# Performance work log

Hardware: AMD Instinct MI355X
Metric: run time of the kernel (lower is better)

## Reference

```python
import jax, jax.numpy as jnp
import numpy as np

B, F, H = 16384, 2048, 4096   # batch, n_features, n_hidden
D, K = 4096, 2048             # num_of_demos, num_of_features


def setup_inputs() -> dict:
    key = jax.random.key(0)
    ks = jax.random.split(key, 16)
    s = 0.02
    return {
        "x": jax.random.normal(ks[0], (B, F), jnp.float32),
        "demo_metric": jax.random.uniform(ks[1], (D, K), jnp.float32),
        "alpha": jax.random.normal(ks[2], (K,), jnp.float32),
        "sample_loss": jax.random.uniform(ks[3], (D, K), jnp.float32),
        "subdom_constant": jax.random.uniform(ks[4], (1,), jnp.float32),
        "num_of_demos": D,
        "num_of_features": K,
        "W1": jax.random.normal(ks[5], (F, H), jnp.float32) * s,
        "b1": jnp.zeros((H,), jnp.float32),
        "W2": jax.random.normal(ks[6], (H, H), jnp.float32) * s,
        "b2": jnp.zeros((H,), jnp.float32),
        "W3": jax.random.normal(ks[7], (H, H), jnp.float32) * s,
        "b3": jnp.zeros((H,), jnp.float32),
        "W4": jax.random.normal(ks[8], (H, 2), jnp.float32) * s,
        "b4": jnp.zeros((2,), jnp.float32),
    }


def reference(x, demo_metric, alpha, sample_loss, subdom_constant,
              num_of_demos, num_of_features,
              W1, b1, W2, b2, W3, b3, W4, b4):
    # subdom hinge loss: max(alpha_k * (sample_loss_jk - demo_loss_jk) + 1, 0) - c
    margin = alpha[None, :] * (sample_loss - demo_metric) + 1.0  # [D, K]
    subdom = jnp.maximum(margin, 0.0) - subdom_constant          # broadcast c
    loss = jnp.sum(subdom)

    # MLP classifier (dropout = identity at inference) + sigmoid
    h = jax.nn.relu(x @ W1 + b1)
    h = jax.nn.relu(h @ W2 + b2)
    h = jax.nn.relu(h @ W3 + b3)
    probs = jax.nn.sigmoid(h @ W4 + b4)  # [B, 2]
    return (loss, probs)
```

## Files before the change

### kernel.cpp

```cpp
#include <hip/hip_runtime.h>
#include <cstdint>
#include <cstddef>

typedef unsigned short u16;
typedef __attribute__((ext_vector_type(8))) __bf16 bf16x8;
typedef __attribute__((ext_vector_type(4))) float f32x4;

__device__ __forceinline__ u16 f2bf(float f) {
  union { float f; unsigned u; } v; v.f = f;
  unsigned r = v.u + 0x7FFFu + ((v.u >> 16) & 1u);
  return (u16)(r >> 16);
}
__device__ __forceinline__ float bf2f(unsigned h) {
  union { unsigned u; float f; } v; v.u = h << 16;
  return v.f;
}

__global__ void init_loss_kernel(const float* __restrict__ c,
                                 const int* __restrict__ D,
                                 const int* __restrict__ K,
                                 float* __restrict__ out) {
  out[0] = -c[0] * (float)D[0] * (float)K[0];
}

__global__ void subdom_kernel(const float4* __restrict__ dm,
                              const float4* __restrict__ sl,
                              const float4* __restrict__ alpha4,
                              float* __restrict__ out, int n4, int k4mask) {
  const int stride = gridDim.x * blockDim.x;
  float s = 0.f;
  for (int i = blockIdx.x * blockDim.x + threadIdx.x; i < n4; i += stride) {
    float4 d = dm[i], l = sl[i], a = alpha4[i & k4mask];
    s += fmaxf(fmaf(a.x, l.x - d.x, 1.f), 0.f);
    s += fmaxf(fmaf(a.y, l.y - d.y, 1.f), 0.f);
    s += fmaxf(fmaf(a.z, l.z - d.z, 1.f), 0.f);
    s += fmaxf(fmaf(a.w, l.w - d.w, 1.f), 0.f);
  }
#pragma unroll
  for (int off = 32; off > 0; off >>= 1) s += __shfl_down(s, off, 64);
  __shared__ float red[4];
  const int lane = threadIdx.x & 63, wave = threadIdx.x >> 6;
  if (lane == 0) red[wave] = s;
  __syncthreads();
  if (threadIdx.x == 0) atomicAdd(out, red[0] + red[1] + red[2] + red[3]);
}

__global__ void cast_f32_bf16_kernel(const float4* __restrict__ in,
                                     u16* __restrict__ out, int n4) {
  const int stride = gridDim.x * blockDim.x;
  for (int i = blockIdx.x * blockDim.x + threadIdx.x; i < n4; i += stride) {
    float4 v = in[i];
    uint2 p;
    p.x = (unsigned)f2bf(v.x) | ((unsigned)f2bf(v.y) << 16);
    p.y = (unsigned)f2bf(v.z) | ((unsigned)f2bf(v.w) << 16);
    ((uint2*)out)[i] = p;
  }
}

__global__ void transpose_cast_kernel(const float* __restrict__ in,
                                      u16* __restrict__ out, int K, int N) {
  __shared__ float tile[32][33];
  const int bx = blockIdx.x * 32;
  const int by = blockIdx.y * 32;
  const int tx = threadIdx.x, ty = threadIdx.y;
#pragma unroll
  for (int i = ty; i < 32; i += 8)
    tile[i][tx] = in[(size_t)(by + i) * N + bx + tx];
  __syncthreads();
#pragma unroll
  for (int i = ty; i < 32; i += 8)
    out[(size_t)(bx + i) * K + by + tx] = f2bf(tile[tx][i]);
}


__device__ __forceinline__ void gload_lds16(const void* g, void* l) {
  __builtin_amdgcn_global_load_lds(
      (const __attribute__((address_space(1))) void*)g,
      (__attribute__((address_space(3))) void*)l, 16, 0, 0);
}

#define VMW(N) asm volatile("s_waitcnt vmcnt(" #N ")" ::: "memory")
#define MF(a, b, c) __builtin_amdgcn_mfma_f32_16x16x32_bf16(a, b, c, 0, 0, 0)

#define STAGE_A(BU, Q, TK)                                                    \
  gload_lds16(A + aGbase + (size_t)((Q)*64) * K + (size_t)(TK)*64,            \
              (void*)(As + ((BU)*4 + (Q)) * 4096 + swave))

#define STAGE_B(BU, NH, HH, TK)                                               \
  gload_lds16(Bt + bGbase + (size_t)((NH)*32 + (HH)*128) * K +                \
                  (size_t)(TK)*64,                                            \
              (void*)(Bs + ((BU)*2 + (NH)) * 8192 + (HH)*4096 + swave))

#define ARD(BU, MH)                                                           \
  {                                                                           \
    const u16* Ar_ = As + ((BU)*4 + wm2 + (MH)) * 4096 + abase;               \
    _Pragma("unroll") for (int f_ = 0; f_ < 4; ++f_) {                        \
      af0[f_] = *(const bf16x8*)(Ar_ + f_ * 1024 + aslot0);                   \
      af1[f_] = *(const bf16x8*)(Ar_ + f_ * 1024 + aslot1);                   \
    }                                                                         \
  }

#define BRD(BF, BU, NH2)                                                      \
  {                                                                           \
    const u16* Br_ = Bs + ((BU)*2 + (NH2)) * 8192 + bbase;                    \
    BF[0] = *(const bf16x8*)(Br_ + aslot0);                                   \
    BF[1] = *(const bf16x8*)(Br_ + aslot1);                                   \
    BF[2] = *(const bf16x8*)(Br_ + 1024 + aslot0);                            \
    BF[3] = *(const bf16x8*)(Br_ + 1024 + aslot1);                            \
  }

#define PH(MH, NH, BF, STAGE_CODE, POST_CODE, WAIT_CODE)                      \
  {                                                                           \
    STAGE_CODE;                                                               \
    __builtin_amdgcn_s_setprio(1);                                            \
    _Pragma("unroll") for (int f_ = 0; f_ < 4; ++f_) {                        \
      acc[(MH)*4 + f_][(NH)*2 + 0] = MF(af0[f_], BF[0], acc[(MH)*4 + f_][(NH)*2 + 0]); \
      acc[(MH)*4 + f_][(NH)*2 + 0] = MF(af1[f_], BF[1], acc[(MH)*4 + f_][(NH)*2 + 0]); \
      acc[(MH)*4 + f_][(NH)*2 + 1] = MF(af0[f_], BF[2], acc[(MH)*4 + f_][(NH)*2 + 1]); \
      acc[(MH)*4 + f_][(NH)*2 + 1] = MF(af1[f_], BF[3], acc[(MH)*4 + f_][(NH)*2 + 1]); \
    }                                                                         \
    __builtin_amdgcn_s_setprio(0);                                            \
    __builtin_amdgcn_sched_barrier(0);                                        \
    POST_CODE;                                                                \
    WAIT_CODE;                                                                \
    __builtin_amdgcn_s_barrier();                                             \
  }

__global__ __launch_bounds__(512, 2) void gemm256(
    const u16* __restrict__ A, const u16* __restrict__ Bt,
    const float* __restrict__ bias, u16* __restrict__ C,
    int M, int N, int K, int act) {
  __shared__ __align__(16) u16 As[2 * 4 * 4096];
  __shared__ __align__(16) u16 Bs[2 * 2 * 8192];

  const int gx = gridDim.x;
  const int bid = blockIdx.x + blockIdx.y * gx;
  const int cpx = (gx * gridDim.y) >> 3;
  const int tilei = (bid & 7) * cpx + (bid >> 3);
  const int m0 = (tilei / gx) * 256;
  const int n0 = (tilei % gx) * 256;

  const int tid = threadIdx.x;
  const int wave = tid >> 6, lane = tid & 63;
  const int l15 = lane & 15, quad = lane >> 4;
  const int wm = wave >> 2, wn = wave & 3;
  const int wm2 = wm << 1;
  const int lsw = l15 & 7;

  const int aslot0 = ((quad ^ lsw) << 3);
  const int aslot1 = (((4 + quad) ^ lsw) << 3);
  const int abase = l15 * 64;
  const int bbase = (wn * 32 + l15) * 64;

  const int srow = tid >> 3;
  const int skch = ((tid & 7) ^ (srow & 7)) << 3;
  const int brow = ((srow >> 5) << 6) + (srow & 31);
  const size_t aGbase = (size_t)(m0 + srow) * K + skch;
  const size_t bGbase = (size_t)(n0 + brow) * K + skch;
  const int swave = wave * 512;

  f32x4 acc[8][4];
#pragma unroll
  for (int i = 0; i < 8; ++i)
#pragma unroll
    for (int j = 0; j < 4; ++j) acc[i][j] = (f32x4){0.f, 0.f, 0.f, 0.f};
  bf16x8 af0[4], af1[4], bfr0[4], bfr1[4];

  STAGE_A(0, 0, 0); STAGE_A(0, 2, 0);
  STAGE_B(0, 0, 0, 0); STAGE_B(0, 0, 1, 0);
  STAGE_B(0, 1, 0, 0); STAGE_B(0, 1, 1, 0);
  STAGE_A(0, 1, 0); STAGE_A(0, 3, 0);
  VMW(2);
  __builtin_amdgcn_s_barrier();
  ARD(0, 0);
  BRD(bfr0, 0, 0);

  const int niter = K >> 7;
  for (int it = 0; it < niter - 1; ++it) {
    const int t1 = 2 * it + 1, t2 = 2 * it + 2;
    PH(0, 0, bfr0,
       { STAGE_A(1, 0, t1); STAGE_A(1, 2, t1);
         STAGE_B(1, 0, 0, t1); STAGE_B(1, 0, 1, t1); },
       { BRD(bfr1, 0, 1); }, { VMW(4); });
    PH(0, 1, bfr1,
       { STAGE_B(1, 1, 0, t1); STAGE_B(1, 1, 1, t1);
         STAGE_A(1, 1, t1); STAGE_A(1, 3, t1); },
       { ARD(0, 1); }, {});
    PH(1, 0, bfr0, {}, {}, { VMW(4); });
    PH(1, 1, bfr1, {}, { ARD(1, 0); BRD(bfr0, 1, 0); }, { VMW(2); });
    PH(0, 0, bfr0,
       { STAGE_A(0, 0, t2); STAGE_A(0, 2, t2);
         STAGE_B(0, 0, 0, t2); STAGE_B(0, 0, 1, t2); },
       { BRD(bfr1, 1, 1); }, { VMW(4); });
    PH(0, 1, bfr1,
       { STAGE_B(0, 1, 0, t2); STAGE_B(0, 1, 1, t2);
         STAGE_A(0, 1, t2); STAGE_A(0, 3, t2); },
       { ARD(1, 1); }, {});
    PH(1, 0, bfr0, {}, {}, { VMW(4); });
    PH(1, 1, bfr1, {}, { ARD(0, 0); BRD(bfr0, 0, 0); }, { VMW(2); });
  }
  {
    const int t1 = 2 * niter - 1;
    PH(0, 0, bfr0,
       { STAGE_A(1, 0, t1); STAGE_A(1, 2, t1);
         STAGE_B(1, 0, 0, t1); STAGE_B(1, 0, 1, t1); },
       { BRD(bfr1, 0, 1); }, { VMW(4); });
    PH(0, 1, bfr1,
       { STAGE_B(1, 1, 0, t1); STAGE_B(1, 1, 1, t1);
         STAGE_A(1, 1, t1); STAGE_A(1, 3, t1); },
       { ARD(0, 1); }, {});
    PH(1, 0, bfr0, {}, {}, { VMW(4); });
    PH(1, 1, bfr1, {}, { ARD(1, 0); BRD(bfr0, 1, 0); }, { VMW(2); });
    PH(0, 0, bfr0, {}, { BRD(bfr1, 1, 1); }, { VMW(0); });
    PH(0, 1, bfr1, {}, { ARD(1, 1); }, {});
    PH(1, 0, bfr0, {}, {}, {});
    PH(1, 1, bfr1, {}, {}, {});
  }

#pragma unroll
  for (int mi = 0; mi < 8; ++mi) {
    const int row = m0 + wm * 128 + (mi >> 2) * 64 + (mi & 3) * 16 + quad * 4;
#pragma unroll
    for (int j = 0; j < 4; ++j) {
      const int col = n0 + wn * 64 + j * 16 + l15;
      const float bv = bias[col];
#pragma unroll
      for (int r = 0; r < 4; ++r) {
        float v = acc[mi][j][r] + bv;
        if (act) v = fmaxf(v, 0.f);
        C[(size_t)(row + r) * N + col] = f2bf(v);
      }
    }
  }
}

__global__ __launch_bounds__(256) void head_kernel(
    const u16* __restrict__ h, const float2* __restrict__ W4,
    const float* __restrict__ b4, float* __restrict__ out, int H) {
  const int row = blockIdx.x;
  const u16* hr = h + (size_t)row * H;
  const int tid = threadIdx.x;
  float p0 = 0.f, p1 = 0.f;
#pragma unroll
  for (int ii = 0; ii < 2; ++ii) {
    const int base = tid * 16 + ii * 8;
    const uint4 hv = *(const uint4*)(hr + base);
    const unsigned uu[4] = {hv.x, hv.y, hv.z, hv.w};
#pragma unroll
    for (int j = 0; j < 4; ++j) {
      float a0 = bf2f(uu[j] & 0xffffu);
      float a1 = bf2f(uu[j] >> 16);
      float2 w0 = W4[base + 2 * j];
      float2 w1 = W4[base + 2 * j + 1];
      p0 += a0 * w0.x + a1 * w1.x;
      p1 += a0 * w0.y + a1 * w1.y;
    }
  }
#pragma unroll
  for (int off = 32; off > 0; off >>= 1) {
    p0 += __shfl_down(p0, off, 64);
    p1 += __shfl_down(p1, off, 64);
  }
  __shared__ float r0[4], r1[4];
  const int lane = tid & 63, wave = tid >> 6;
  if (lane == 0) { r0[wave] = p0; r1[wave] = p1; }
  __syncthreads();
  if (tid == 0) {
    float l0 = r0[0] + r0[1] + r0[2] + r0[3] + b4[0];
    float l1 = r1[0] + r1[1] + r1[2] + r1[3] + b4[1];
    out[1 + row * 2] = 1.f / (1.f + __expf(-l0));
    out[2 + row * 2] = 1.f / (1.f + __expf(-l1));
  }
}

extern "C" void kernel_launch(void* const* d_in, const int* in_sizes, int n_in,
                              void* d_out, int out_size, void* d_ws,
                              size_t ws_size, hipStream_t stream) {
  (void)in_sizes; (void)n_in; (void)out_size; (void)ws_size;
  const float* x  = (const float*)d_in[0];
  const float* dm = (const float*)d_in[1];
  const float* al = (const float*)d_in[2];
  const float* sl = (const float*)d_in[3];
  const float* sc = (const float*)d_in[4];
  const int*   nd = (const int*)d_in[5];
  const int*   nf = (const int*)d_in[6];
  const float* W1 = (const float*)d_in[7];
  const float* b1 = (const float*)d_in[8];
  const float* W2 = (const float*)d_in[9];
  const float* b2 = (const float*)d_in[10];
  const float* W3 = (const float*)d_in[11];
  const float* b3 = (const float*)d_in[12];
  const float* W4 = (const float*)d_in[13];
  const float* b4 = (const float*)d_in[14];
  float* out = (float*)d_out;

  const int B = 16384, F = 2048, H = 4096, D = 4096, K = 2048;

  char* ws = (char*)d_ws;
  u16* xb = (u16*)ws;
  u16* wt = (u16*)(ws + (size_t)B * F * 2);
  u16* hA = (u16*)(ws + (size_t)B * F * 2 + (size_t)H * H * 2);
  u16* hB = hA + (size_t)B * H;

  init_loss_kernel<<<1, 1, 0, stream>>>(sc, nd, nf, out);
  subdom_kernel<<<1024, 256, 0, stream>>>((const float4*)dm, (const float4*)sl,
                                          (const float4*)al, out, D * K / 4,
                                          K / 4 - 1);
  cast_f32_bf16_kernel<<<4096, 256, 0, stream>>>((const float4*)x, xb, B * F / 4);
  transpose_cast_kernel<<<dim3(H / 32, F / 32), dim3(32, 8), 0, stream>>>(W1, wt, F, H);
  gemm256<<<dim3(H / 256, B / 256), 512, 0, stream>>>(xb, wt, b1, hA, B, H, F, 1);
  transpose_cast_kernel<<<dim3(H / 32, H / 32), dim3(32, 8), 0, stream>>>(W2, wt, H, H);
  gemm256<<<dim3(H / 256, B / 256), 512, 0, stream>>>(hA, wt, b2, hB, B, H, H, 1);
  transpose_cast_kernel<<<dim3(H / 32, H / 32), dim3(32, 8), 0, stream>>>(W3, wt, H, H);
  gemm256<<<dim3(H / 256, B / 256), 512, 0, stream>>>(hB, wt, b3, hA, B, H, H, 1);
  head_kernel<<<B, 256, 0, stream>>>(hA, (const float2*)W4, b4, out, H);
}
```

Baseline: 1.879 ms.

## Restructure GEMM main loop into four 32-MFMA phases with deeper B prefetch

```diff
diff --git a/kernel.cpp b/kernel.cpp
--- a/kernel.cpp
+++ b/kernel.cpp
@@ -109,22 +109,19 @@
     BF[3] = *(const bf16x8*)(Br_ + 1024 + aslot1);                            \
   }
 
-#define PH(MH, NH, BF, STAGE_CODE, POST_CODE, WAIT_CODE)                      \
-  {                                                                           \
-    STAGE_CODE;                                                               \
-    __builtin_amdgcn_s_setprio(1);                                            \
-    _Pragma("unroll") for (int f_ = 0; f_ < 4; ++f_) {                        \
-      acc[(MH)*4 + f_][(NH)*2 + 0] = MF(af0[f_], BF[0], acc[(MH)*4 + f_][(NH)*2 + 0]); \
-      acc[(MH)*4 + f_][(NH)*2 + 0] = MF(af1[f_], BF[1], acc[(MH)*4 + f_][(NH)*2 + 0]); \
-      acc[(MH)*4 + f_][(NH)*2 + 1] = MF(af0[f_], BF[2], acc[(MH)*4 + f_][(NH)*2 + 1]); \
-      acc[(MH)*4 + f_][(NH)*2 + 1] = MF(af1[f_], BF[3], acc[(MH)*4 + f_][(NH)*2 + 1]); \
-    }                                                                         \
-    __builtin_amdgcn_s_setprio(0);                                            \
-    __builtin_amdgcn_sched_barrier(0);                                        \
-    POST_CODE;                                                                \
-    WAIT_CODE;                                                                \
-    __builtin_amdgcn_s_barrier();                                             \
-  }
+#define MFMA32(MH)                                                            \
+  __builtin_amdgcn_s_setprio(1);                                              \
+  _Pragma("unroll") for (int f_ = 0; f_ < 4; ++f_) {                          \
+    acc[(MH)*4 + f_][0] = MF(af0[f_], bfr0[0], acc[(MH)*4 + f_][0]);          \
+    acc[(MH)*4 + f_][0] = MF(af1[f_], bfr0[1], acc[(MH)*4 + f_][0]);          \
+    acc[(MH)*4 + f_][1] = MF(af0[f_], bfr0[2], acc[(MH)*4 + f_][1]);          \
+    acc[(MH)*4 + f_][1] = MF(af1[f_], bfr0[3], acc[(MH)*4 + f_][1]);          \
+    acc[(MH)*4 + f_][2] = MF(af0[f_], bfr1[0], acc[(MH)*4 + f_][2]);          \
+    acc[(MH)*4 + f_][2] = MF(af1[f_], bfr1[1], acc[(MH)*4 + f_][2]);          \
+    acc[(MH)*4 + f_][3] = MF(af0[f_], bfr1[2], acc[(MH)*4 + f_][3]);          \
+    acc[(MH)*4 + f_][3] = MF(af1[f_], bfr1[3], acc[(MH)*4 + f_][3]);          \
+  }                                                                           \
+  __builtin_amdgcn_s_setprio(0);
 
 __global__ __launch_bounds__(512, 2) void gemm256(
     const u16* __restrict__ A, const u16* __restrict__ Bt,
@@ -170,51 +167,46 @@
   STAGE_B(0, 0, 0, 0); STAGE_B(0, 0, 1, 0);
   STAGE_B(0, 1, 0, 0); STAGE_B(0, 1, 1, 0);
   STAGE_A(0, 1, 0); STAGE_A(0, 3, 0);
-  VMW(2);
+  STAGE_B(1, 0, 0, 1); STAGE_B(1, 0, 1, 1);
+  STAGE_B(1, 1, 0, 1); STAGE_B(1, 1, 1, 1);
+  VMW(6);
   __builtin_amdgcn_s_barrier();
-  ARD(0, 0);
-  BRD(bfr0, 0, 0);
 
   const int niter = K >> 7;
-  for (int it = 0; it < niter - 1; ++it) {
-    const int t1 = 2 * it + 1, t2 = 2 * it + 2;
-    PH(0, 0, bfr0,
-       { STAGE_A(1, 0, t1); STAGE_A(1, 2, t1);
-         STAGE_B(1, 0, 0, t1); STAGE_B(1, 0, 1, t1); },
-       { BRD(bfr1, 0, 1); }, { VMW(4); });
-    PH(0, 1, bfr1,
-       { STAGE_B(1, 1, 0, t1); STAGE_B(1, 1, 1, t1);
-         STAGE_A(1, 1, t1); STAGE_A(1, 3, t1); },
-       { ARD(0, 1); }, {});
-    PH(1, 0, bfr0, {}, {}, { VMW(4); });
-    PH(1, 1, bfr1, {}, { ARD(1, 0); BRD(bfr0, 1, 0); }, { VMW(2); });
-    PH(0, 0, bfr0,
-       { STAGE_A(0, 0, t2); STAGE_A(0, 2, t2);
-         STAGE_B(0, 0, 0, t2); STAGE_B(0, 0, 1, t2); },
-       { BRD(bfr1, 1, 1); }, { VMW(4); });
-    PH(0, 1, bfr1,
-       { STAGE_B(0, 1, 0, t2); STAGE_B(0, 1, 1, t2);
-         STAGE_A(0, 1, t2); STAGE_A(0, 3, t2); },
-       { ARD(1, 1); }, {});
-    PH(1, 0, bfr0, {}, {}, { VMW(4); });
-    PH(1, 1, bfr1, {}, { ARD(0, 0); BRD(bfr0, 0, 0); }, { VMW(2); });
-  }
-  {
-    const int t1 = 2 * niter - 1;
-    PH(0, 0, bfr0,
-       { STAGE_A(1, 0, t1); STAGE_A(1, 2, t1);
-         STAGE_B(1, 0, 0, t1); STAGE_B(1, 0, 1, t1); },
-       { BRD(bfr1, 0, 1); }, { VMW(4); });
-    PH(0, 1, bfr1,
-       { STAGE_B(1, 1, 0, t1); STAGE_B(1, 1, 1, t1);
-         STAGE_A(1, 1, t1); STAGE_A(1, 3, t1); },
-       { ARD(0, 1); }, {});
-    PH(1, 0, bfr0, {}, {}, { VMW(4); });
-    PH(1, 1, bfr1, {}, { ARD(1, 0); BRD(bfr0, 1, 0); }, { VMW(2); });
-    PH(0, 0, bfr0, {}, { BRD(bfr1, 1, 1); }, { VMW(0); });
-    PH(0, 1, bfr1, {}, { ARD(1, 1); }, {});
-    PH(1, 0, bfr0, {}, {}, {});
-    PH(1, 1, bfr1, {}, {}, {});
+  for (int it = 0; it < niter; ++it) {
+    const int t1 = 2 * it + 1, t2 = 2 * it + 2, t3 = 2 * it + 3;
+    const bool nl = (it + 1 < niter);
+    BRD(bfr0, 0, 0);
+    ARD(0, 0);
+    BRD(bfr1, 0, 1);
+    STAGE_A(1, 0, t1); STAGE_A(1, 2, t1);
+    STAGE_A(1, 1, t1); STAGE_A(1, 3, t1);
+    MFMA32(0);
+    VMW(8);
+    __builtin_amdgcn_s_barrier();
+    ARD(0, 1);
+    MFMA32(1);
+    VMW(0);
+    __builtin_amdgcn_s_barrier();
+    BRD(bfr0, 1, 0);
+    ARD(1, 0);
+    BRD(bfr1, 1, 1);
+    if (nl) {
+      STAGE_B(0, 0, 0, t2); STAGE_B(0, 0, 1, t2);
+      STAGE_B(0, 1, 0, t2); STAGE_B(0, 1, 1, t2);
+      STAGE_A(0, 0, t2); STAGE_A(0, 2, t2);
+    }
+    MFMA32(0);
+    __builtin_amdgcn_s_barrier();
+    ARD(1, 1);
+    if (nl) {
+      STAGE_A(0, 1, t2); STAGE_A(0, 3, t2);
+      STAGE_B(1, 0, 0, t3); STAGE_B(1, 0, 1, t3);
+      STAGE_B(1, 1, 0, t3); STAGE_B(1, 1, 1, t3);
+    }
+    MFMA32(1);
+    VMW(6);
+    __builtin_amdgcn_s_barrier();
   }
 
 #pragma unroll
```

Measured after the change: 1.529 ms. 1.23x faster.
